# Performance work log

Measured on AMD Instinct MI355X. Metric: run time of the kernel, lower is better.

## Reference

```python
import jax, jax.numpy as jnp
import numpy as np

N, E = 50000, 800000
NODE_DIM, EDGE_DIM = 96, 64
IN_DIM = 2 * NODE_DIM + EDGE_DIM  # 256


def setup_inputs() -> dict:
    key = jax.random.key(0)
    k = jax.random.split(key, 7)
    h = jax.random.normal(k[0], (N, NODE_DIM), dtype=jnp.float32)
    edge_index = jax.random.randint(k[1], (2, E), 0, N, dtype=jnp.int64)
    edge_attr = jax.random.normal(k[2], (E, EDGE_DIM), dtype=jnp.float32)
    # Linear params (PyTorch default-ish scale)
    s = 1.0 / np.sqrt(IN_DIM)
    W_e = jax.random.uniform(k[3], (IN_DIM, NODE_DIM), jnp.float32, -s, s)
    b_e = jax.random.uniform(k[4], (NODE_DIM,), jnp.float32, -s, s)
    W_n = jax.random.uniform(k[5], (IN_DIM, NODE_DIM), jnp.float32, -s, s)
    b_n = jax.random.uniform(k[6], (NODE_DIM,), jnp.float32, -s, s)
    return {"h": h, "edge_index": edge_index, "edge_attr": edge_attr,
            "W_e": W_e, "b_e": b_e, "W_n": W_n, "b_n": b_n}


def reference(h, edge_index, edge_attr, W_e, b_e, W_n, b_n):
    src, dst = edge_index[0], edge_index[1]
    concat = jnp.concatenate([h[src], h[dst], edge_attr], axis=-1)  # [E, 256]
    gates = jax.nn.sigmoid(concat @ W_e + b_e)                      # [E, node_dim]
    messages = jax.nn.softplus(concat @ W_n + b_n)                  # [E, node_dim]
    gated = gates * messages
    n = h.shape[0]
    h_new = jax.ops.segment_sum(gated, dst, num_segments=n)         # [N, node_dim]
    edge_count = jax.ops.segment_sum(jnp.ones((dst.shape[0],), h.dtype), dst, num_segments=n)
    edge_count = jnp.clip(edge_count, 1.0, None)[:, None]
    return h + h_new / edge_count
```

## Files before the change

kernel.cpp:

```cpp
#include <hip/hip_runtime.h>
#include <hip/hip_bf16.h>


#define NODE_DIM 96
#define EDGE_DIM 64
#define IN_DIM   256
#define TILE_E   64
#define NT_TILES 12
#define KT_TILES 8
#define A_STRIDE 272

typedef float  f32x4  __attribute__((ext_vector_type(4)));
typedef __bf16 bf16x8 __attribute__((ext_vector_type(8)));

__device__ __forceinline__ unsigned short bf16rne(float f) {
    unsigned int u = __float_as_uint(f);
    u += 0x7FFFu + ((u >> 16) & 1u);
    return (unsigned short)(u >> 16);
}

__global__ void pack_w_kernel(const float* __restrict__ We,
                              const float* __restrict__ Wn,
                              unsigned short* __restrict__ bpack) {
    int t = blockIdx.x * blockDim.x + threadIdx.x;
    if (t >= KT_TILES * NT_TILES * 64) return;
    int tile = t >> 6, lane = t & 63;
    int kt = tile / NT_TILES, nt = tile % NT_TILES;
    const float* W = (nt < 6) ? We : Wn;
    int n  = (nt % 6) * 16 + (lane & 15);
    int k0 = kt * 32 + (lane >> 4) * 8;
    union { unsigned short u[8]; uint4 v; } tmp;
#pragma unroll
    for (int j = 0; j < 8; ++j) tmp.u[j] = bf16rne(W[(k0 + j) * NODE_DIM + n]);
    *(uint4*)(bpack + (size_t)t * 8) = tmp.v;
}

__global__ __launch_bounds__(256)
void cgconv_main_kernel(const float* __restrict__ h,
                        const int*   __restrict__ eidx,
                        const float* __restrict__ ea,
                        const unsigned short* __restrict__ bpack,
                        const float* __restrict__ be,
                        const float* __restrict__ bn,
                        float* __restrict__ hnew,
                        float* __restrict__ cnt,
                        int E) {
    __shared__ unsigned short sA[TILE_E][A_STRIDE];
    __shared__ int s_src[TILE_E];
    __shared__ int s_dst[TILE_E];

    const int tid = threadIdx.x;
    const int e0  = blockIdx.x * TILE_E;

    if (tid < TILE_E) {
        int e = e0 + tid;
        int s = 0, d = -1;
        if (e < E) {
            s = eidx[e];
            d = eidx[E + e];
            unsafeAtomicAdd(cnt + d, 1.0f);
        }
        s_src[tid] = s;
        s_dst[tid] = d;
    }
    __syncthreads();

    for (int idx = tid; idx < TILE_E * 24; idx += 256) {
        int e = idx / 24, q = idx - e * 24;
        const float4 v = *(const float4*)(h + (size_t)s_src[e] * NODE_DIM + q * 4);
        union { unsigned short u[4]; uint2 w; } p;
        p.u[0] = bf16rne(v.x); p.u[1] = bf16rne(v.y);
        p.u[2] = bf16rne(v.z); p.u[3] = bf16rne(v.w);
        *(uint2*)&sA[e][q * 4] = p.w;
    }
    for (int idx = tid; idx < TILE_E * 24; idx += 256) {
        int e = idx / 24, q = idx - e * 24;
        int d = s_dst[e]; if (d < 0) d = 0;
        const float4 v = *(const float4*)(h + (size_t)d * NODE_DIM + q * 4);
        union { unsigned short u[4]; uint2 w; } p;
        p.u[0] = bf16rne(v.x); p.u[1] = bf16rne(v.y);
        p.u[2] = bf16rne(v.z); p.u[3] = bf16rne(v.w);
        *(uint2*)&sA[e][NODE_DIM + q * 4] = p.w;
    }
    for (int idx = tid; idx < TILE_E * 16; idx += 256) {
        int e = idx >> 4, q = idx & 15;
        size_t ee = (size_t)(e0 + e);
        if (e0 + e >= E) ee = (size_t)e0;
        const float4 v = *(const float4*)(ea + ee * EDGE_DIM + q * 4);
        union { unsigned short u[4]; uint2 w; } p;
        p.u[0] = bf16rne(v.x); p.u[1] = bf16rne(v.y);
        p.u[2] = bf16rne(v.z); p.u[3] = bf16rne(v.w);
        *(uint2*)&sA[e][2 * NODE_DIM + q * 4] = p.w;
    }
    __syncthreads();

    const int wave = tid >> 6, lane = tid & 63;
    const int lrow = lane & 15, lquad = lane >> 4;

    f32x4 acc[NT_TILES];
#pragma unroll
    for (int nt = 0; nt < NT_TILES; ++nt) acc[nt] = (f32x4){0.f, 0.f, 0.f, 0.f};

    const unsigned short* aBase = &sA[wave * 16 + lrow][0];
#pragma unroll
    for (int kt = 0; kt < KT_TILES; ++kt) {
        bf16x8 afrag = *(const bf16x8*)(aBase + kt * 32 + lquad * 8);
#pragma unroll
        for (int nt = 0; nt < NT_TILES; ++nt) {
            bf16x8 bfrag = *(const bf16x8*)(bpack +
                             (size_t)((kt * NT_TILES + nt) * 64 + lane) * 8);
            acc[nt] = __builtin_amdgcn_mfma_f32_16x16x32_bf16(afrag, bfrag, acc[nt], 0, 0, 0);
        }
    }

#pragma unroll
    for (int nt = 0; nt < 6; ++nt) {
        const int col = nt * 16 + lrow;
        const float bev = be[col];
        const float bnv = bn[col];
#pragma unroll
        for (int r = 0; r < 4; ++r) {
            const int row = wave * 16 + lquad * 4 + r;
            const int d = s_dst[row];
            if (d < 0) continue;
            float g = acc[nt][r] + bev;
            float m = acc[nt + 6][r] + bnv;
            float gate = 1.0f / (1.0f + __expf(-g));
            float sp   = fmaxf(m, 0.0f) + __logf(1.0f + __expf(-fabsf(m)));
            unsafeAtomicAdd(hnew + (size_t)d * NODE_DIM + col, gate * sp);
        }
    }
}

__global__ void finalize_kernel(const float* __restrict__ h,
                                const float* __restrict__ hnew,
                                const float* __restrict__ cnt,
                                float* __restrict__ out,
                                int total4) {
    int i = blockIdx.x * blockDim.x + threadIdx.x;
    if (i >= total4) return;
    int n = i / 24;
    float c = fmaxf(cnt[n], 1.0f);
    float inv = 1.0f / c;
    float4 hv = ((const float4*)h)[i];
    float4 av = ((const float4*)hnew)[i];
    float4 o;
    o.x = hv.x + av.x * inv;
    o.y = hv.y + av.y * inv;
    o.z = hv.z + av.z * inv;
    o.w = hv.w + av.w * inv;
    ((float4*)out)[i] = o;
}

extern "C" void kernel_launch(void* const* d_in, const int* in_sizes, int n_in,
                              void* d_out, int out_size, void* d_ws, size_t ws_size,
                              hipStream_t stream) {
    const float* h   = (const float*)d_in[0];
    const int*   ei  = (const int*)  d_in[1];
    const float* ea  = (const float*)d_in[2];
    const float* We  = (const float*)d_in[3];
    const float* be  = (const float*)d_in[4];
    const float* Wn  = (const float*)d_in[5];
    const float* bn  = (const float*)d_in[6];

    const int N = in_sizes[0] / NODE_DIM;
    const int E = in_sizes[2] / EDGE_DIM;

    char* ws = (char*)d_ws;
    const size_t BPACK_BYTES = (size_t)KT_TILES * NT_TILES * 64 * 8 * 2;
    const size_t CNT_OFF  = BPACK_BYTES;
    const size_t HNEW_OFF = CNT_OFF + (((size_t)N * 4 + 511) / 512) * 512;
    const size_t HNEW_BYTES = (size_t)N * NODE_DIM * 4;

    unsigned short* bpack = (unsigned short*)ws;
    float* cnt  = (float*)(ws + CNT_OFF);
    float* hnew = (float*)(ws + HNEW_OFF);

    hipMemsetAsync(ws + CNT_OFF, 0, HNEW_OFF - CNT_OFF + HNEW_BYTES, stream);

    pack_w_kernel<<<(KT_TILES * NT_TILES * 64 + 255) / 256, 256, 0, stream>>>(We, Wn, bpack);

    const int nblk = (E + TILE_E - 1) / TILE_E;
    cgconv_main_kernel<<<nblk, 256, 0, stream>>>(h, ei, ea, bpack, be, bn, hnew, cnt, E);

    const int total4 = N * (NODE_DIM / 4);
    finalize_kernel<<<(total4 + 255) / 256, 256, 0, stream>>>(h, hnew, cnt, (float*)d_out, total4);
}
```

Baseline: 749.4 us.

## Load MFMA A fragments directly from global memory, dropping the LDS staging tile

Removes the shared-memory A tile and both block barriers. Each lane now gathers its own edge's h[src], h[dst] and edge_attr slice straight from global memory, converts it to bf16 in registers and feeds it to the MFMA. Destination indices are broadcast with wave shuffles, and launch bounds request 4 blocks per SIMD to raise occupancy. The trade-off is less coalesced global loads, since each lane reads 32-byte chunks from scattered rows, and possible register pressure under the new launch bound.

```diff
diff --git a/kernel.cpp b/kernel.cpp
--- a/kernel.cpp
+++ b/kernel.cpp
@@ -8,7 +8,6 @@
 #define TILE_E   64
 #define NT_TILES 12
 #define KT_TILES 8
-#define A_STRIDE 272
 
 typedef float  f32x4  __attribute__((ext_vector_type(4)));
 typedef __bf16 bf16x8 __attribute__((ext_vector_type(8)));
@@ -35,7 +34,7 @@
     *(uint4*)(bpack + (size_t)t * 8) = tmp.v;
 }
 
-__global__ __launch_bounds__(256)
+__global__ __launch_bounds__(256, 4)
 void cgconv_main_kernel(const float* __restrict__ h,
                         const int*   __restrict__ eidx,
                         const float* __restrict__ ea,
@@ -45,89 +44,67 @@
                         float* __restrict__ hnew,
                         float* __restrict__ cnt,
                         int E) {
-    __shared__ unsigned short sA[TILE_E][A_STRIDE];
-    __shared__ int s_src[TILE_E];
-    __shared__ int s_dst[TILE_E];
+    const int tid  = threadIdx.x;
+    const int wave = tid >> 6, lane = tid & 63;
+    const int m    = lane & 15;
+    const int quad = lane >> 4;
 
-    const int tid = threadIdx.x;
-    const int e0  = blockIdx.x * TILE_E;
+    const int e  = blockIdx.x * TILE_E + wave * 16 + m;
+    const int eg = (e < E) ? e : (E - 1);
+    const int src = eidx[eg];
+    const int dst = eidx[E + eg];
 
-    if (tid < TILE_E) {
-        int e = e0 + tid;
-        int s = 0, d = -1;
-        if (e < E) {
-            s = eidx[e];
-            d = eidx[E + e];
-            unsafeAtomicAdd(cnt + d, 1.0f);
-        }
-        s_src[tid] = s;
-        s_dst[tid] = d;
-    }
-    __syncthreads();
-
-    for (int idx = tid; idx < TILE_E * 24; idx += 256) {
-        int e = idx / 24, q = idx - e * 24;
-        const float4 v = *(const float4*)(h + (size_t)s_src[e] * NODE_DIM + q * 4);
-        union { unsigned short u[4]; uint2 w; } p;
-        p.u[0] = bf16rne(v.x); p.u[1] = bf16rne(v.y);
-        p.u[2] = bf16rne(v.z); p.u[3] = bf16rne(v.w);
-        *(uint2*)&sA[e][q * 4] = p.w;
-    }
-    for (int idx = tid; idx < TILE_E * 24; idx += 256) {
-        int e = idx / 24, q = idx - e * 24;
-        int d = s_dst[e]; if (d < 0) d = 0;
-        const float4 v = *(const float4*)(h + (size_t)d * NODE_DIM + q * 4);
-        union { unsigned short u[4]; uint2 w; } p;
-        p.u[0] = bf16rne(v.x); p.u[1] = bf16rne(v.y);
-        p.u[2] = bf16rne(v.z); p.u[3] = bf16rne(v.w);
-        *(uint2*)&sA[e][NODE_DIM + q * 4] = p.w;
-    }
-    for (int idx = tid; idx < TILE_E * 16; idx += 256) {
-        int e = idx >> 4, q = idx & 15;
-        size_t ee = (size_t)(e0 + e);
-        if (e0 + e >= E) ee = (size_t)e0;
-        const float4 v = *(const float4*)(ea + ee * EDGE_DIM + q * 4);
-        union { unsigned short u[4]; uint2 w; } p;
-        p.u[0] = bf16rne(v.x); p.u[1] = bf16rne(v.y);
-        p.u[2] = bf16rne(v.z); p.u[3] = bf16rne(v.w);
-        *(uint2*)&sA[e][2 * NODE_DIM + q * 4] = p.w;
-    }
-    __syncthreads();
-
-    const int wave = tid >> 6, lane = tid & 63;
-    const int lrow = lane & 15, lquad = lane >> 4;
+    if (quad == 0 && e < E) unsafeAtomicAdd(cnt + dst, 1.0f);
 
     f32x4 acc[NT_TILES];
 #pragma unroll
     for (int nt = 0; nt < NT_TILES; ++nt) acc[nt] = (f32x4){0.f, 0.f, 0.f, 0.f};
 
-    const unsigned short* aBase = &sA[wave * 16 + lrow][0];
+    const float* hsrc = h + (size_t)src * NODE_DIM;
+    const float* hdst = h + (size_t)dst * NODE_DIM;
+    const float* earo = ea + (size_t)eg * EDGE_DIM;
+
 #pragma unroll
     for (int kt = 0; kt < KT_TILES; ++kt) {
-        bf16x8 afrag = *(const bf16x8*)(aBase + kt * 32 + lquad * 8);
+        const int ko = kt * 32 + quad * 8;
+        const float* p;
+        if (kt < 3)      p = hsrc + ko;
+        else if (kt < 6) p = hdst + (ko - NODE_DIM);
+        else             p = earo + (ko - 2 * NODE_DIM);
+        const float4 v0 = *(const float4*)p;
+        const float4 v1 = *(const float4*)(p + 4);
+        union { unsigned short u[8]; bf16x8 b; } A;
+        A.u[0] = bf16rne(v0.x); A.u[1] = bf16rne(v0.y);
+        A.u[2] = bf16rne(v0.z); A.u[3] = bf16rne(v0.w);
+        A.u[4] = bf16rne(v1.x); A.u[5] = bf16rne(v1.y);
+        A.u[6] = bf16rne(v1.z); A.u[7] = bf16rne(v1.w);
 #pragma unroll
         for (int nt = 0; nt < NT_TILES; ++nt) {
             bf16x8 bfrag = *(const bf16x8*)(bpack +
                              (size_t)((kt * NT_TILES + nt) * 64 + lane) * 8);
-            acc[nt] = __builtin_amdgcn_mfma_f32_16x16x32_bf16(afrag, bfrag, acc[nt], 0, 0, 0);
+            acc[nt] = __builtin_amdgcn_mfma_f32_16x16x32_bf16(A.b, bfrag, acc[nt], 0, 0, 0);
         }
     }
 
+    int drow[4], erow[4];
+#pragma unroll
+    for (int r = 0; r < 4; ++r) {
+        drow[r] = __shfl(dst, quad * 4 + r, 64);
+        erow[r] = blockIdx.x * TILE_E + wave * 16 + quad * 4 + r;
+    }
 #pragma unroll
     for (int nt = 0; nt < 6; ++nt) {
-        const int col = nt * 16 + lrow;
+        const int col = nt * 16 + m;
         const float bev = be[col];
         const float bnv = bn[col];
 #pragma unroll
         for (int r = 0; r < 4; ++r) {
-            const int row = wave * 16 + lquad * 4 + r;
-            const int d = s_dst[row];
-            if (d < 0) continue;
-            float g = acc[nt][r] + bev;
-            float m = acc[nt + 6][r] + bnv;
+            if (erow[r] >= E) continue;
+            float g  = acc[nt][r] + bev;
+            float mm = acc[nt + 6][r] + bnv;
             float gate = 1.0f / (1.0f + __expf(-g));
-            float sp   = fmaxf(m, 0.0f) + __logf(1.0f + __expf(-fabsf(m)));
-            unsafeAtomicAdd(hnew + (size_t)d * NODE_DIM + col, gate * sp);
+            float sp   = fmaxf(mm, 0.0f) + __logf(1.0f + __expf(-fabsf(mm)));
+            unsafeAtomicAdd(hnew + (size_t)drow[r] * NODE_DIM + col, gate * sp);
         }
     }
 }
```

New measurement: 738.6 us. About the same (-1.4%).
